# Performance work log

Hardware: AMD Instinct MI355X
Metric: run time of the kernel (lower is better)

Reference implementation:

```python
import jax, jax.numpy as jnp
import numpy as np

Q, P = 32, 32          # output / input channels per node
N1, N2 = 64, 64        # per-dimension quadrature grid sizes (d = 2)
B = 16                 # batch
HID = 128              # MLP hidden width (kernel_layers = [128, 128])


def _mlp_K(y, x, Ws, bs):
    """Per-dimension NN kernel: K[a, c, i, j] = MLP([y_i, x_j])[a*P + c].

    Returns the Khatri-Rao component of shape (Q, P, n_out, n_in).
    """
    n_out, n_in = y.shape[0], x.shape[0]
    feats = jnp.stack([jnp.broadcast_to(y[:, None], (n_out, n_in)),
                       jnp.broadcast_to(x[None, :], (n_out, n_in))], axis=-1)  # (n_out, n_in, 2)
    h = feats
    for W, b in zip(Ws[:-1], bs[:-1]):
        h = jax.nn.gelu(h @ W + b)
    out = h @ Ws[-1] + bs[-1]  # (n_out, n_in, Q*P)
    return out.reshape(n_out, n_in, Q, P).transpose(2, 3, 0, 1)


def setup_inputs() -> dict:
    key = jax.random.key(0)
    ks = jax.random.split(key, 12)

    def w(k, shape):
        return jax.random.normal(k, shape, jnp.float32) / np.float32(np.sqrt(shape[0]))

    return {
        "u":  jax.random.normal(ks[0], (B, P * N1 * N2), jnp.float32),
        "x1": jax.random.uniform(ks[1], (N1,), jnp.float32),   # quadrature points dim 1
        "x2": jax.random.uniform(ks[2], (N2,), jnp.float32),   # quadrature points dim 2
        "w1": jax.random.uniform(ks[3], (N1,), jnp.float32) / N1,  # quadrature weights dim 1
        "w2": jax.random.uniform(ks[4], (N2,), jnp.float32) / N2,  # quadrature weights dim 2
        "k1_W0": w(ks[5], (2, HID)),    "k1_b0": jnp.zeros((HID,), jnp.float32),
        "k1_W1": w(ks[6], (HID, HID)),  "k1_b1": jnp.zeros((HID,), jnp.float32),
        "k1_W2": w(ks[7], (HID, Q * P)), "k1_b2": jnp.zeros((Q * P,), jnp.float32),
        "k2_W0": w(ks[8], (2, HID)),    "k2_b0": jnp.zeros((HID,), jnp.float32),
        "k2_W1": w(ks[9], (HID, HID)),  "k2_b1": jnp.zeros((HID,), jnp.float32),
        "k2_W2": w(ks[10], (HID, Q * P)), "k2_b2": jnp.zeros((Q * P,), jnp.float32),
    }


def reference(u, x1, x2, w1, w2,
              k1_W0, k1_b0, k1_W1, k1_b1, k1_W2, k1_b2,
              k2_W0, k2_b0, k2_W1, k2_b1, k2_W2, k2_b2):
    # Khatri-Rao components, one per spatial dimension
    K1 = _mlp_K(x1, x1, [k1_W0, k1_W1, k1_W2], [k1_b0, k1_b1, k1_b2])  # (Q, P, N1, N1)
    K2 = _mlp_K(x2, x2, [k2_W0, k2_W1, k2_W2], [k2_b0, k2_b1, k2_b2])  # (Q, P, N2, N2)

    # (I_p kron diag(w1 kron w2)) @ u^T  ==  per-channel quadrature weighting
    v = u.reshape(B, P, N1, N2)
    vw = v * w1[None, None, :, None] * w2[None, None, None, :]

    # Block (a, c) of the full kernel is K1[a, c] kron K2[a, c]; apply it as two
    # mode-products without ever materializing the (Q*N, P*N) dense matrix.
    Z1 = jnp.einsum('acij,bcjm->bacim', K1, vw)    # contract dim-1 input index j
    out = jnp.einsum('ackm,bacim->baik', K2, Z1)   # contract dim-2 index m, sum channels c
    return out.reshape(B, Q * N1 * N2)
```

## Files before the change

### kernel.cpp

```cpp
#include <hip/hip_runtime.h>
#include <cmath>

namespace {

typedef short short8 __attribute__((ext_vector_type(8)));
typedef float f32x4  __attribute__((ext_vector_type(4)));
typedef unsigned short ushort;

constexpr int HID  = 128;
constexpr int QP   = 1024;
constexpr int N    = 64;
constexpr int NPTS = 4096;
constexpr int B    = 16;
constexpr int P    = 32;
constexpr int Q    = 32;
constexpr int LDH  = 136;
constexpr int CH   = 4;
constexpr int CCH  = P / CH;

__device__ __forceinline__ ushort f2bf(float x) {
    unsigned u = __float_as_uint(x);
    u += 0x7FFF + ((u >> 16) & 1);
    return (ushort)(u >> 16);
}
__device__ __forceinline__ float bf2f(ushort b) {
    return __uint_as_float((unsigned)b << 16);
}
__device__ __forceinline__ float gelu_tanh(float x) {
    const float c0 = 0.7978845608028654f;
    const float c1 = 0.044715f;
    float inner = c0 * (x + c1 * x * x * x);
    return 0.5f * x * (1.0f + tanhf(inner));
}
__device__ __forceinline__ void gll16(const ushort* src, ushort* dst) {
    __builtin_amdgcn_global_load_lds(
        (const __attribute__((address_space(1))) unsigned int*)src,
        (__attribute__((address_space(3))) unsigned int*)dst, 16, 0, 0);
}

__global__ __launch_bounds__(256)
void prep_kernel(const float* __restrict__ W1a, const float* __restrict__ W2a,
                 const float* __restrict__ W1b, const float* __restrict__ W2b,
                 const float* __restrict__ u,
                 ushort* __restrict__ W1Th, ushort* __restrict__ W1Tl,
                 ushort* __restrict__ W2Th, ushort* __restrict__ W2Tl,
                 ushort* __restrict__ ubf)
{
    const int bid = blockIdx.x;
    if (bid < 1152) {
        const int g   = bid * 256 + threadIdx.x;
        const int dim = g / 147456;
        const int r   = g - dim * 147456;
        const float* W1 = dim ? W1b : W1a;
        const float* W2 = dim ? W2b : W2a;
        float v; ushort *dh, *dl; int idx;
        if (r < 16384) {
            const int o = r >> 7, k = r & 127;
            v = W1[k * HID + o];
            idx = dim * 16384 + r;
            dh = W1Th; dl = W1Tl;
        } else {
            const int r2 = r - 16384;
            const int o = r2 >> 7, k = r2 & 127;
            v = W2[k * QP + o];
            idx = dim * 131072 + r2;
            dh = W2Th; dl = W2Tl;
        }
        const ushort h = f2bf(v);
        const ushort l = f2bf(v - bf2f(h));
        dh[idx] = h; dl[idx] = l;
    } else {
        const int g = (bid - 1152) * 256 + threadIdx.x;
        const float4 v = reinterpret_cast<const float4*>(u)[g];
        uint2 pk;
        pk.x = (unsigned)f2bf(v.x) | ((unsigned)f2bf(v.y) << 16);
        pk.y = (unsigned)f2bf(v.z) | ((unsigned)f2bf(v.w) << 16);
        reinterpret_cast<uint2*>(ubf)[g] = pk;
    }
}

__global__ __launch_bounds__(256, 1)
void mlp_kernel(const float* __restrict__ xs1, const float* __restrict__ xs2,
                const float* __restrict__ W0a, const float* __restrict__ b0a,
                const float* __restrict__ b1a, const float* __restrict__ b2a,
                const float* __restrict__ W0b, const float* __restrict__ b0b,
                const float* __restrict__ b1b, const float* __restrict__ b2b,
                const ushort* __restrict__ W1Th, const ushort* __restrict__ W1Tl,
                const ushort* __restrict__ W2Th, const ushort* __restrict__ W2Tl,
                const float* __restrict__ qw1, const float* __restrict__ qw2,
                ushort* __restrict__ K1out, ushort* __restrict__ K2out)
{
    __shared__ ushort h0h[N * LDH], h0l[N * LDH];
    __shared__ ushort h1h[N * LDH], h1l[N * LDH];

    const int i   = blockIdx.x;
    const int dim = blockIdx.y;
    const int bz  = blockIdx.z;
    const float* xs = dim ? xs2 : xs1;
    const float* W0 = dim ? W0b : W0a;
    const float* b0 = dim ? b0b : b0a;
    const float* b1 = dim ? b1b : b1a;
    const float* b2 = dim ? b2b : b2a;
    const float* wq = dim ? qw2 : qw1;
    const ushort* w1h = W1Th + dim * 16384;
    const ushort* w1l = W1Tl + dim * 16384;
    const ushort* w2h = W2Th + dim * 131072;
    const ushort* w2l = W2Tl + dim * 131072;
    ushort* Kout = dim ? K2out : K1out;

    const int t  = threadIdx.x;
    const int w  = t >> 6;
    const int l  = t & 63;
    const int lr = l & 15;
    const int lh = l >> 4;
    const float y = xs[i];

    {
        const int ch    = t & 127;
        const int pbase = (t >> 7) * 32;
        const float wy = W0[ch], wx = W0[HID + ch], bb = b0[ch];
        for (int pp = 0; pp < 32; ++pp) {
            const int pt = pbase + pp;
            const float z = fmaf(y, wy, fmaf(xs[pt], wx, bb));
            const float h = gelu_tanh(z);
            const ushort hb = f2bf(h);
            h0h[pt * LDH + ch] = hb;
            h0l[pt * LDH + ch] = f2bf(h - bf2f(hb));
        }
    }
    __syncthreads();

    {
        #pragma unroll
        for (int cc = 0; cc < 2; ++cc) {
            const int ct = w * 2 + cc;
            const ushort* ap = w1h + (ct * 16 + lr) * HID + lh * 8;
            const ushort* aq = w1l + (ct * 16 + lr) * HID + lh * 8;
            short8 Ah[4], Al[4];
            #pragma unroll
            for (int kk = 0; kk < 4; ++kk) {
                Ah[kk] = *reinterpret_cast<const short8*>(ap + kk * 32);
                Al[kk] = *reinterpret_cast<const short8*>(aq + kk * 32);
            }
            f32x4 acc[4];
            #pragma unroll
            for (int p = 0; p < 4; ++p) acc[p] = f32x4{0.f, 0.f, 0.f, 0.f};
            #pragma unroll
            for (int kk = 0; kk < 4; ++kk) {
                short8 Bh[4], Bl[4];
                #pragma unroll
                for (int p = 0; p < 4; ++p) {
                    Bh[p] = *reinterpret_cast<const short8*>(&h0h[(p * 16 + lr) * LDH + kk * 32 + lh * 8]);
                    Bl[p] = *reinterpret_cast<const short8*>(&h0l[(p * 16 + lr) * LDH + kk * 32 + lh * 8]);
                }
                #pragma unroll
                for (int p = 0; p < 4; ++p)
                    acc[p] = __builtin_amdgcn_mfma_f32_16x16x32_bf16(Ah[kk], Bh[p], acc[p], 0, 0, 0);
                #pragma unroll
                for (int p = 0; p < 4; ++p)
                    acc[p] = __builtin_amdgcn_mfma_f32_16x16x32_bf16(Al[kk], Bh[p], acc[p], 0, 0, 0);
                #pragma unroll
                for (int p = 0; p < 4; ++p)
                    acc[p] = __builtin_amdgcn_mfma_f32_16x16x32_bf16(Ah[kk], Bl[p], acc[p], 0, 0, 0);
            }
            const float4 bb = *reinterpret_cast<const float4*>(&b1[ct * 16 + lh * 4]);
            #pragma unroll
            for (int p = 0; p < 4; ++p) {
                ushort hb[4], lb[4];
                #pragma unroll
                for (int r = 0; r < 4; ++r) {
                    const float zv = acc[p][r] + ((const float*)&bb)[r];
                    const float h  = gelu_tanh(zv);
                    hb[r] = f2bf(h);
                    lb[r] = f2bf(h - bf2f(hb[r]));
                }
                uint2 ph, pl;
                ph.x = (unsigned)hb[0] | ((unsigned)hb[1] << 16);
                ph.y = (unsigned)hb[2] | ((unsigned)hb[3] << 16);
                pl.x = (unsigned)lb[0] | ((unsigned)lb[1] << 16);
                pl.y = (unsigned)lb[2] | ((unsigned)lb[3] << 16);
                const int off = (p * 16 + lr) * LDH + ct * 16 + lh * 4;
                *reinterpret_cast<uint2*>(&h1h[off]) = ph;
                *reinterpret_cast<uint2*>(&h1l[off]) = pl;
            }
        }
    }
    __syncthreads();

    {
        short8 Ah[4][4], Al[4][4];
        #pragma unroll
        for (int p = 0; p < 4; ++p)
            #pragma unroll
            for (int kk = 0; kk < 4; ++kk) {
                Ah[p][kk] = *reinterpret_cast<const short8*>(&h1h[(p * 16 + lr) * LDH + kk * 32 + lh * 8]);
                Al[p][kk] = *reinterpret_cast<const short8*>(&h1l[(p * 16 + lr) * LDH + kk * 32 + lh * 8]);
            }

        const int otbase = bz * 32 + w * 8;

#define LOADB(BH, BL, OT) do {                                                      \
        const ushort* _p = w2h + (size_t)((OT) * 16 + lr) * HID + lh * 8;           \
        const ushort* _q = w2l + (size_t)((OT) * 16 + lr) * HID + lh * 8;           \
        _Pragma("unroll")                                                           \
        for (int kk = 0; kk < 4; ++kk) {                                            \
            BH[kk] = *reinterpret_cast<const short8*>(_p + kk * 32);                \
            BL[kk] = *reinterpret_cast<const short8*>(_q + kk * 32);                \
        } } while (0)

#define MMTILE(BH, BL, OT) do {                                                     \
        f32x4 acc[4];                                                               \
        _Pragma("unroll")                                                           \
        for (int p = 0; p < 4; ++p) acc[p] = f32x4{0.f, 0.f, 0.f, 0.f};             \
        _Pragma("unroll")                                                           \
        for (int kk = 0; kk < 4; ++kk) {                                            \
            _Pragma("unroll")                                                       \
            for (int p = 0; p < 4; ++p)                                             \
                acc[p] = __builtin_amdgcn_mfma_f32_16x16x32_bf16(Ah[p][kk], BH[kk], acc[p], 0, 0, 0); \
            _Pragma("unroll")                                                       \
            for (int p = 0; p < 4; ++p)                                             \
                acc[p] = __builtin_amdgcn_mfma_f32_16x16x32_bf16(Al[p][kk], BH[kk], acc[p], 0, 0, 0); \
            _Pragma("unroll")                                                       \
            for (int p = 0; p < 4; ++p)                                             \
                acc[p] = __builtin_amdgcn_mfma_f32_16x16x32_bf16(Ah[p][kk], BL[kk], acc[p], 0, 0, 0); \
        }                                                                           \
        const int _o = (OT) * 16 + lr;                                              \
        const float _bo = b2[_o];                                                   \
        ushort* _d = Kout + (size_t)_o * NPTS + i * 64 + lh * 4;                    \
        _Pragma("unroll")                                                           \
        for (int p = 0; p < 4; ++p) {                                               \
            const float4 _wv = *reinterpret_cast<const float4*>(wq + p * 16 + lh * 4); \
            uint2 pk;                                                               \
            pk.x = (unsigned)f2bf((acc[p][0] + _bo) * _wv.x) |                      \
                   ((unsigned)f2bf((acc[p][1] + _bo) * _wv.y) << 16);               \
            pk.y = (unsigned)f2bf((acc[p][2] + _bo) * _wv.z) |                      \
                   ((unsigned)f2bf((acc[p][3] + _bo) * _wv.w) << 16);               \
            *reinterpret_cast<uint2*>(_d + p * 16) = pk;                            \
        } } while (0)

        short8 B0h[4], B0l[4], B1h[4], B1l[4];
        LOADB(B0h, B0l, otbase + 0);
        #pragma unroll
        for (int oo = 0; oo < 8; oo += 2) {
            if (oo + 1 < 8) LOADB(B1h, B1l, otbase + oo + 1);
            MMTILE(B0h, B0l, otbase + oo);
            if (oo + 2 < 8) LOADB(B0h, B0l, otbase + oo + 2);
            MMTILE(B1h, B1l, otbase + oo + 1);
        }
#undef LOADB
#undef MMTILE
    }
}

__global__ __launch_bounds__(256, 2)
void contract_kernel(const ushort* __restrict__ ubf,
                     const ushort* __restrict__ K1,
                     const ushort* __restrict__ K2,
                     float* __restrict__ part)
{
    __shared__ ushort sK1[2][4096];
    __shared__ ushort sK2[2][4096];
    __shared__ ushort sZT[4][4096];

    const int id0 = blockIdx.x;
    const int id  = (id0 & 7) * 64 + (id0 >> 3);
    const int bg  = id & 3;
    const int a   = (id >> 2) & 31;
    const int ch  = id >> 7;

    const int t  = threadIdx.x;
    const int w  = t >> 6;
    const int l  = t & 63;
    const int lr = l & 15;
    const int lh = l >> 4;
    const int b  = bg * 4 + w;
    const int c0 = ch * CCH;

    ushort* zt = &sZT[w][0];
    const int sc = (((l & 7) ^ (l >> 3)) << 3);
    const int r0 = 16 * w + (l >> 3);

#define STAGE(NB, CC) do {                                                      \
        const ushort* _k1 = K1 + (((size_t)a * P + (CC)) << 12);                \
        const ushort* _k2 = K2 + (((size_t)a * P + (CC)) << 12);                \
        gll16(_k1 + (r0    ) * 64 + sc, &sK1[NB][w * 1024      ]);              \
        gll16(_k1 + (r0 + 8) * 64 + sc, &sK1[NB][w * 1024 + 512]);              \
        gll16(_k2 + (r0    ) * 64 + sc, &sK2[NB][w * 1024      ]);              \
        gll16(_k2 + (r0 + 8) * 64 + sc, &sK2[NB][w * 1024 + 512]);              \
    } while (0)

#define LOAD_UF(UF, CC) do {                                                    \
        const ushort* _up = ubf + (((size_t)b * P + (CC)) << 12);               \
        _Pragma("unroll")                                                       \
        for (int jt = 0; jt < 4; ++jt)                                          \
            _Pragma("unroll")                                                   \
            for (int kk = 0; kk < 2; ++kk)                                      \
                UF[jt][kk] = *reinterpret_cast<const short8*>(                  \
                    _up + (16 * jt + lr) * 64 + kk * 32 + lh * 8);              \
    } while (0)

#define MM1(BUF, UF) do {                                                       \
        short8 Bf[4][2];                                                        \
        _Pragma("unroll")                                                       \
        for (int kt = 0; kt < 4; ++kt)                                          \
            _Pragma("unroll")                                                   \
            for (int kk = 0; kk < 2; ++kk)                                      \
                Bf[kt][kk] = *reinterpret_cast<const short8*>(                  \
                    &sK2[BUF][(16 * kt + lr) * 64 + (((kk * 4 + lh) ^ (lr & 7)) << 3)]); \
        _Pragma("unroll")                                                       \
        for (int jt = 0; jt < 4; ++jt)                                          \
            _Pragma("unroll")                                                   \
            for (int kt = 0; kt < 4; ++kt) zacc[jt][kt] = f32x4{0.f, 0.f, 0.f, 0.f}; \
        __builtin_amdgcn_s_setprio(1);                                          \
        _Pragma("unroll")                                                       \
        for (int kk = 0; kk < 2; ++kk)                                          \
            _Pragma("unroll")                                                   \
            for (int jt = 0; jt < 4; ++jt)                                      \
                _Pragma("unroll")                                               \
                for (int kt = 0; kt < 4; ++kt)                                  \
                    zacc[jt][kt] = __builtin_amdgcn_mfma_f32_16x16x32_bf16(     \
                        UF[jt][kk], Bf[kt][kk], zacc[jt][kt], 0, 0, 0);         \
        __builtin_amdgcn_s_setprio(0);                                          \
    } while (0)

#define ZTW() do {                                                              \
        _Pragma("unroll")                                                       \
        for (int kt = 0; kt < 4; ++kt) {                                        \
            const int rbase = (16 * kt + lr) * 64;                              \
            _Pragma("unroll")                                                   \
            for (int jt = 0; jt < 4; ++jt) {                                    \
                const f32x4 z = zacc[jt][kt];                                   \
                uint2 pk;                                                       \
                pk.x = (unsigned)f2bf(z[0]) | ((unsigned)f2bf(z[1]) << 16);     \
                pk.y = (unsigned)f2bf(z[2]) | ((unsigned)f2bf(z[3]) << 16);     \
                const int g = (2 * jt + (lh >> 1)) ^ (lr & 7);                  \
                *reinterpret_cast<uint2*>(&zt[rbase + (g << 3) + (lh & 1) * 4]) = pk; \
            }                                                                   \
        }                                                                       \
    } while (0)

#define MM2(BUF) do {                                                           \
        _Pragma("unroll")                                                       \
        for (int jj = 0; jj < 2; ++jj) {                                        \
            short8 A2[4], B2[4];                                                \
            _Pragma("unroll")                                                   \
            for (int it = 0; it < 4; ++it)                                      \
                A2[it] = *reinterpret_cast<const short8*>(                      \
                    &sK1[BUF][(16 * it + lr) * 64 + (((jj * 4 + lh) ^ (lr & 7)) << 3)]); \
            _Pragma("unroll")                                                   \
            for (int kt = 0; kt < 4; ++kt)                                      \
                B2[kt] = *reinterpret_cast<const short8*>(                      \
                    &zt[(16 * kt + lr) * 64 + (((jj * 4 + lh) ^ (lr & 7)) << 3)]); \
            __builtin_amdgcn_s_setprio(1);                                      \
            _Pragma("unroll")                                                   \
            for (int it = 0; it < 4; ++it)                                      \
                _Pragma("unroll")                                               \
                for (int kt = 0; kt < 4; ++kt)                                  \
                    oacc[it][kt] = __builtin_amdgcn_mfma_f32_16x16x32_bf16(     \
                        A2[it], B2[kt], oacc[it][kt], 0, 0, 0);                 \
            __builtin_amdgcn_s_setprio(0);                                      \
        }                                                                       \
    } while (0)

    f32x4 oacc[4][4];
    #pragma unroll
    for (int it = 0; it < 4; ++it)
        #pragma unroll
        for (int kt = 0; kt < 4; ++kt) oacc[it][kt] = f32x4{0.f, 0.f, 0.f, 0.f};
    f32x4 zacc[4][4];
    short8 UFa[4][2], UFb[4][2];

    STAGE(0, c0);
    LOAD_UF(UFa, c0);
    __syncthreads();

    #pragma unroll
    for (int cc = 0; cc < CCH; ++cc) {
        const int cur = cc & 1;
        if (cc + 1 < CCH) STAGE(cur ^ 1, c0 + cc + 1);
        if (cur == 0) {
            MM1(0, UFa);
            if (cc + 1 < CCH) LOAD_UF(UFb, c0 + cc + 1);
        } else {
            MM1(1, UFb);
            if (cc + 1 < CCH) LOAD_UF(UFa, c0 + cc + 1);
        }
        ZTW();
        asm volatile("s_waitcnt lgkmcnt(0)" ::: "memory");
        __builtin_amdgcn_sched_barrier(0);
        MM2(cur);
        __syncthreads();
    }

#undef STAGE
#undef LOAD_UF
#undef MM1
#undef ZTW
#undef MM2

    float* pp = part + ((((size_t)ch * B + b) * Q + a) << 12);
    #pragma unroll
    for (int it = 0; it < 4; ++it)
        #pragma unroll
        for (int kt = 0; kt < 4; ++kt)
            #pragma unroll
            for (int r = 0; r < 4; ++r)
                pp[(16 * it + 4 * lh + r) * 64 + 16 * kt + lr] = oacc[it][kt][r];
}

__global__ __launch_bounds__(256)
void addparts_kernel(const float* __restrict__ part, float* __restrict__ out)
{
    const int g = blockIdx.x * 256 + threadIdx.x;
    constexpr size_t SLAB = (size_t)B * Q * NPTS / 4;
    const float4* p = reinterpret_cast<const float4*>(part);
    float4 s0 = p[g];
    float4 s1 = p[g + SLAB];
    float4 s2 = p[g + 2 * SLAB];
    float4 s3 = p[g + 3 * SLAB];
    float4 r;
    r.x = (s0.x + s1.x) + (s2.x + s3.x);
    r.y = (s0.y + s1.y) + (s2.y + s3.y);
    r.z = (s0.z + s1.z) + (s2.z + s3.z);
    r.w = (s0.w + s1.w) + (s2.w + s3.w);
    reinterpret_cast<float4*>(out)[g] = r;
}

}

extern "C" void kernel_launch(void* const* d_in, const int* in_sizes, int n_in,
                              void* d_out, int out_size, void* d_ws, size_t ws_size,
                              hipStream_t stream)
{
    const float* u     = (const float*)d_in[0];
    const float* x1    = (const float*)d_in[1];
    const float* x2    = (const float*)d_in[2];
    const float* w1    = (const float*)d_in[3];
    const float* w2    = (const float*)d_in[4];
    const float* k1W0  = (const float*)d_in[5];
    const float* k1b0  = (const float*)d_in[6];
    const float* k1W1  = (const float*)d_in[7];
    const float* k1b1  = (const float*)d_in[8];
    const float* k1W2  = (const float*)d_in[9];
    const float* k1b2  = (const float*)d_in[10];
    const float* k2W0  = (const float*)d_in[11];
    const float* k2b0  = (const float*)d_in[12];
    const float* k2W1  = (const float*)d_in[13];
    const float* k2b1  = (const float*)d_in[14];
    const float* k2W2  = (const float*)d_in[15];
    const float* k2b2  = (const float*)d_in[16];

    float* out = (float*)d_out;
    char* ws = (char*)d_ws;
    size_t off = 0;
    ushort* K1buf = (ushort*)(ws + off); off += (size_t)QP * NPTS * 2;
    ushort* K2buf = (ushort*)(ws + off); off += (size_t)QP * NPTS * 2;
    ushort* W2Th  = (ushort*)(ws + off); off += 2 * 131072 * 2;
    ushort* W2Tl  = (ushort*)(ws + off); off += 2 * 131072 * 2;
    ushort* W1Th  = (ushort*)(ws + off); off += 2 * 16384 * 2;
    ushort* W1Tl  = (ushort*)(ws + off); off += 2 * 16384 * 2;
    ushort* ubf   = (ushort*)(ws + off); off += (size_t)B * P * NPTS * 2;
    float*  part  = (float*)(ws + off);  off += (size_t)CH * B * Q * NPTS * 4;

    prep_kernel<<<dim3(3200), 256, 0, stream>>>(
        k1W1, k1W2, k2W1, k2W2, u, W1Th, W1Tl, W2Th, W2Tl, ubf);

    mlp_kernel<<<dim3(64, 2, 2), 256, 0, stream>>>(
        x1, x2,
        k1W0, k1b0, k1b1, k1b2,
        k2W0, k2b0, k2b1, k2b2,
        W1Th, W1Tl, W2Th, W2Tl,
        w1, w2,
        K1buf, K2buf);

    contract_kernel<<<dim3(512), 256, 0, stream>>>(ubf, K1buf, K2buf, part);

    addparts_kernel<<<dim3((B * Q * NPTS) / (256 * 4)), 256, 0, stream>>>(part, out);
}
```

Measured before the change: 67.12 us.

## Repartition MLP kernel grid over input points and store partial sums as bf16

The MLP kernel now splits each row's 64 input points into two halves across blockIdx.z instead of splitting output tiles. Each block then recomputes layer 1 for only 32 points and runs all output tiles, with a smaller LDS footprint and an occupancy hint of two blocks per CU. Separately, the contract kernel writes its per-chunk partial sums as bf16 instead of fp32, halving the partial buffer traffic, and the reduction kernel unpacks and sums eight elements per thread. This trades accuracy in the partial sums for less memory traffic, and makes each MLP block reload the full W2 slice.

```diff
diff --git a/kernel.cpp b/kernel.cpp
--- a/kernel.cpp
+++ b/kernel.cpp
@@ -79,7 +79,7 @@
     }
 }
 
-__global__ __launch_bounds__(256, 1)
+__global__ __launch_bounds__(256, 2)
 void mlp_kernel(const float* __restrict__ xs1, const float* __restrict__ xs2,
                 const float* __restrict__ W0a, const float* __restrict__ b0a,
                 const float* __restrict__ b1a, const float* __restrict__ b2a,
@@ -90,12 +90,12 @@
                 const float* __restrict__ qw1, const float* __restrict__ qw2,
                 ushort* __restrict__ K1out, ushort* __restrict__ K2out)
 {
-    __shared__ ushort h0h[N * LDH], h0l[N * LDH];
-    __shared__ ushort h1h[N * LDH], h1l[N * LDH];
+    __shared__ ushort h0h[32 * LDH], h0l[32 * LDH];
+    __shared__ ushort h1h[32 * LDH], h1l[32 * LDH];
 
     const int i   = blockIdx.x;
     const int dim = blockIdx.y;
-    const int bz  = blockIdx.z;
+    const int jh  = blockIdx.z;
     const float* xs = dim ? xs2 : xs1;
     const float* W0 = dim ? W0b : W0a;
     const float* b0 = dim ? b0b : b0a;
@@ -117,11 +117,11 @@
 
     {
         const int ch    = t & 127;
-        const int pbase = (t >> 7) * 32;
+        const int pbase = (t >> 7) * 16;
         const float wy = W0[ch], wx = W0[HID + ch], bb = b0[ch];
-        for (int pp = 0; pp < 32; ++pp) {
+        for (int pp = 0; pp < 16; ++pp) {
             const int pt = pbase + pp;
-            const float z = fmaf(y, wy, fmaf(xs[pt], wx, bb));
+            const float z = fmaf(y, wy, fmaf(xs[jh * 32 + pt], wx, bb));
             const float h = gelu_tanh(z);
             const ushort hb = f2bf(h);
             h0h[pt * LDH + ch] = hb;
@@ -142,30 +142,30 @@
                 Ah[kk] = *reinterpret_cast<const short8*>(ap + kk * 32);
                 Al[kk] = *reinterpret_cast<const short8*>(aq + kk * 32);
             }
-            f32x4 acc[4];
-            #pragma unroll
-            for (int p = 0; p < 4; ++p) acc[p] = f32x4{0.f, 0.f, 0.f, 0.f};
+            f32x4 acc[2];
+            #pragma unroll
+            for (int p = 0; p < 2; ++p) acc[p] = f32x4{0.f, 0.f, 0.f, 0.f};
             #pragma unroll
             for (int kk = 0; kk < 4; ++kk) {
-                short8 Bh[4], Bl[4];
+                short8 Bh[2], Bl[2];
                 #pragma unroll
-                for (int p = 0; p < 4; ++p) {
+                for (int p = 0; p < 2; ++p) {
                     Bh[p] = *reinterpret_cast<const short8*>(&h0h[(p * 16 + lr) * LDH + kk * 32 + lh * 8]);
                     Bl[p] = *reinterpret_cast<const short8*>(&h0l[(p * 16 + lr) * LDH + kk * 32 + lh * 8]);
                 }
                 #pragma unroll
-                for (int p = 0; p < 4; ++p)
+                for (int p = 0; p < 2; ++p)
                     acc[p] = __builtin_amdgcn_mfma_f32_16x16x32_bf16(Ah[kk], Bh[p], acc[p], 0, 0, 0);
                 #pragma unroll
-                for (int p = 0; p < 4; ++p)
+                for (int p = 0; p < 2; ++p)
                     acc[p] = __builtin_amdgcn_mfma_f32_16x16x32_bf16(Al[kk], Bh[p], acc[p], 0, 0, 0);
                 #pragma unroll
-                for (int p = 0; p < 4; ++p)
+                for (int p = 0; p < 2; ++p)
                     acc[p] = __builtin_amdgcn_mfma_f32_16x16x32_bf16(Ah[kk], Bl[p], acc[p], 0, 0, 0);
             }
             const float4 bb = *reinterpret_cast<const float4*>(&b1[ct * 16 + lh * 4]);
             #pragma unroll
-            for (int p = 0; p < 4; ++p) {
+            for (int p = 0; p < 2; ++p) {
                 ushort hb[4], lb[4];
                 #pragma unroll
                 for (int r = 0; r < 4; ++r) {
@@ -188,16 +188,16 @@
     __syncthreads();
 
     {
-        short8 Ah[4][4], Al[4][4];
+        short8 Ah[2][4], Al[2][4];
         #pragma unroll
-        for (int p = 0; p < 4; ++p)
+        for (int p = 0; p < 2; ++p)
             #pragma unroll
             for (int kk = 0; kk < 4; ++kk) {
                 Ah[p][kk] = *reinterpret_cast<const short8*>(&h1h[(p * 16 + lr) * LDH + kk * 32 + lh * 8]);
                 Al[p][kk] = *reinterpret_cast<const short8*>(&h1l[(p * 16 + lr) * LDH + kk * 32 + lh * 8]);
             }
 
-        const int otbase = bz * 32 + w * 8;
+        const int otbase = w * 16;
 
 #define LOADB(BH, BL, OT) do {                                                      \
         const ushort* _p = w2h + (size_t)((OT) * 16 + lr) * HID + lh * 8;           \
@@ -209,27 +209,27 @@
         } } while (0)
 
 #define MMTILE(BH, BL, OT) do {                                                     \
-        f32x4 acc[4];                                                               \
+        f32x4 acc[2];                                                               \
         _Pragma("unroll")                                                           \
-        for (int p = 0; p < 4; ++p) acc[p] = f32x4{0.f, 0.f, 0.f, 0.f};             \
+        for (int p = 0; p < 2; ++p) acc[p] = f32x4{0.f, 0.f, 0.f, 0.f};             \
         _Pragma("unroll")                                                           \
         for (int kk = 0; kk < 4; ++kk) {                                            \
             _Pragma("unroll")                                                       \
-            for (int p = 0; p < 4; ++p)                                             \
+            for (int p = 0; p < 2; ++p)                                             \
                 acc[p] = __builtin_amdgcn_mfma_f32_16x16x32_bf16(Ah[p][kk], BH[kk], acc[p], 0, 0, 0); \
             _Pragma("unroll")                                                       \
-            for (int p = 0; p < 4; ++p)                                             \
+            for (int p = 0; p < 2; ++p)                                             \
                 acc[p] = __builtin_amdgcn_mfma_f32_16x16x32_bf16(Al[p][kk], BH[kk], acc[p], 0, 0, 0); \
             _Pragma("unroll")                                                       \
-            for (int p = 0; p < 4; ++p)                                             \
+            for (int p = 0; p < 2; ++p)                                             \
                 acc[p] = __builtin_amdgcn_mfma_f32_16x16x32_bf16(Ah[p][kk], BL[kk], acc[p], 0, 0, 0); \
         }                                                                           \
         const int _o = (OT) * 16 + lr;                                              \
         const float _bo = b2[_o];                                                   \
-        ushort* _d = Kout + (size_t)_o * NPTS + i * 64 + lh * 4;                    \
+        ushort* _d = Kout + (size_t)_o * NPTS + i * 64 + jh * 32 + lh * 4;          \
         _Pragma("unroll")                                                           \
-        for (int p = 0; p < 4; ++p) {                                               \
-            const float4 _wv = *reinterpret_cast<const float4*>(wq + p * 16 + lh * 4); \
+        for (int p = 0; p < 2; ++p) {                                               \
+            const float4 _wv = *reinterpret_cast<const float4*>(wq + jh * 32 + p * 16 + lh * 4); \
             uint2 pk;                                                               \
             pk.x = (unsigned)f2bf((acc[p][0] + _bo) * _wv.x) |                      \
                    ((unsigned)f2bf((acc[p][1] + _bo) * _wv.y) << 16);               \
@@ -241,10 +241,10 @@
         short8 B0h[4], B0l[4], B1h[4], B1l[4];
         LOADB(B0h, B0l, otbase + 0);
         #pragma unroll
-        for (int oo = 0; oo < 8; oo += 2) {
-            if (oo + 1 < 8) LOADB(B1h, B1l, otbase + oo + 1);
+        for (int oo = 0; oo < 16; oo += 2) {
+            if (oo + 1 < 16) LOADB(B1h, B1l, otbase + oo + 1);
             MMTILE(B0h, B0l, otbase + oo);
-            if (oo + 2 < 8) LOADB(B0h, B0l, otbase + oo + 2);
+            if (oo + 2 < 16) LOADB(B0h, B0l, otbase + oo + 2);
             MMTILE(B1h, B1l, otbase + oo + 1);
         }
 #undef LOADB
@@ -256,7 +256,7 @@
 void contract_kernel(const ushort* __restrict__ ubf,
                      const ushort* __restrict__ K1,
                      const ushort* __restrict__ K2,
-                     float* __restrict__ part)
+                     ushort* __restrict__ part)
 {
     __shared__ ushort sK1[2][4096];
     __shared__ ushort sK2[2][4096];
@@ -398,32 +398,39 @@
 #undef ZTW
 #undef MM2
 
-    float* pp = part + ((((size_t)ch * B + b) * Q + a) << 12);
+    ushort* pp = part + ((((size_t)ch * B + b) * Q + a) << 12);
     #pragma unroll
     for (int it = 0; it < 4; ++it)
         #pragma unroll
         for (int kt = 0; kt < 4; ++kt)
             #pragma unroll
             for (int r = 0; r < 4; ++r)
-                pp[(16 * it + 4 * lh + r) * 64 + 16 * kt + lr] = oacc[it][kt][r];
+                pp[(16 * it + 4 * lh + r) * 64 + 16 * kt + lr] = f2bf(oacc[it][kt][r]);
 }
 
 __global__ __launch_bounds__(256)
-void addparts_kernel(const float* __restrict__ part, float* __restrict__ out)
+void addparts_kernel(const ushort* __restrict__ part, float* __restrict__ out)
 {
     const int g = blockIdx.x * 256 + threadIdx.x;
-    constexpr size_t SLAB = (size_t)B * Q * NPTS / 4;
-    const float4* p = reinterpret_cast<const float4*>(part);
-    float4 s0 = p[g];
-    float4 s1 = p[g + SLAB];
-    float4 s2 = p[g + 2 * SLAB];
-    float4 s3 = p[g + 3 * SLAB];
-    float4 r;
-    r.x = (s0.x + s1.x) + (s2.x + s3.x);
-    r.y = (s0.y + s1.y) + (s2.y + s3.y);
-    r.z = (s0.z + s1.z) + (s2.z + s3.z);
-    r.w = (s0.w + s1.w) + (s2.w + s3.w);
-    reinterpret_cast<float4*>(out)[g] = r;
+    constexpr size_t SLAB = (size_t)B * Q * NPTS / 8;
+    const uint4* p = reinterpret_cast<const uint4*>(part);
+    const uint4 s0 = p[g];
+    const uint4 s1 = p[g + SLAB];
+    const uint4 s2 = p[g + 2 * SLAB];
+    const uint4 s3 = p[g + 3 * SLAB];
+    float r[8];
+    #pragma unroll
+    for (int e = 0; e < 8; ++e) {
+        const int wd = e >> 1, sh = (e & 1) * 16;
+        const float v0 = bf2f((ushort)(((const unsigned*)&s0)[wd] >> sh));
+        const float v1 = bf2f((ushort)(((const unsigned*)&s1)[wd] >> sh));
+        const float v2 = bf2f((ushort)(((const unsigned*)&s2)[wd] >> sh));
+        const float v3 = bf2f((ushort)(((const unsigned*)&s3)[wd] >> sh));
+        r[e] = (v0 + v1) + (v2 + v3);
+    }
+    float4* o = reinterpret_cast<float4*>(out);
+    o[g * 2]     = make_float4(r[0], r[1], r[2], r[3]);
+    o[g * 2 + 1] = make_float4(r[4], r[5], r[6], r[7]);
 }
 
 }
@@ -460,7 +467,7 @@
     ushort* W1Th  = (ushort*)(ws + off); off += 2 * 16384 * 2;
     ushort* W1Tl  = (ushort*)(ws + off); off += 2 * 16384 * 2;
     ushort* ubf   = (ushort*)(ws + off); off += (size_t)B * P * NPTS * 2;
-    float*  part  = (float*)(ws + off);  off += (size_t)CH * B * Q * NPTS * 4;
+    ushort* part  = (ushort*)(ws + off); off += (size_t)CH * B * Q * NPTS * 2;
 
     prep_kernel<<<dim3(3200), 256, 0, stream>>>(
         k1W1, k1W2, k2W1, k2W2, u, W1Th, W1Tl, W2Th, W2Tl, ubf);
@@ -475,5 +482,5 @@
 
     contract_kernel<<<dim3(512), 256, 0, stream>>>(ubf, K1buf, K2buf, part);
 
-    addparts_kernel<<<dim3((B * Q * NPTS) / (256 * 4)), 256, 0, stream>>>(part, out);
-}
+    addparts_kernel<<<dim3((B * Q * NPTS) / (256 * 8)), 256, 0, stream>>>(part, out);
+}
```

Result: no change. 68.19 us (+1.6%).
